# Kernel tuning notes

Hardware: AMD Instinct MI355X
Metric: run time of the kernel (lower is better)

The kernel has to match this reference:

```python
import jax, jax.numpy as jnp
import numpy as np

BETA = 0.25


def setup_inputs() -> dict:
    key = jax.random.key(0)
    k1, k2 = jax.random.split(key)
    inputs = jax.random.normal(k1, (16, 64, 64, 256), dtype=jnp.float32)
    # codebook, shape (embedding_dim=256, num_embeddings=1024), uniform init like tf
    embeddings = jax.random.uniform(k2, (256, 1024), dtype=jnp.float32)
    return {"inputs": inputs, "embeddings": embeddings}


def reference(inputs, embeddings):
    D = embeddings.shape[0]
    flat = inputs.reshape(-1, D)  # [N, D]
    distances = (
        jnp.sum(flat * flat, axis=1, keepdims=True)
        - 2.0 * (flat @ embeddings)
        + jnp.sum(embeddings * embeddings, axis=0, keepdims=True)
    )
    encoding_indices = jnp.argmin(distances, axis=1)  # == argmax(-d)
    # one_hot @ embeddings.T is just a row gather from the codebook
    quantized = jnp.take(embeddings.T, encoding_indices, axis=0).reshape(inputs.shape)
    commitment_loss = BETA * jnp.mean(
        (jax.lax.stop_gradient(quantized) - inputs) ** 2
    )
    # straight-through estimator
    quantized = inputs + jax.lax.stop_gradient(quantized - inputs)
    return quantized, commitment_loss, encoding_indices
```

## Files before the change

kernel.cpp:

```cpp
#include <hip/hip_runtime.h>
#include <float.h>

typedef _Float16 half8 __attribute__((ext_vector_type(8)));
typedef float    f32x4 __attribute__((ext_vector_type(4)));
typedef unsigned long long u64;

#define N_ROWS   65536
#define DIM      256
#define KCODES   1024
#define VQ_BETA  0.25
#define MARGIN   1.5f
#define HCAP     640

__device__ __forceinline__ unsigned fkey(float f) {
    const unsigned u = __float_as_uint(f);
    return u ^ (0x80000000u | (unsigned)((int)u >> 31));
}

__global__ void transpose_e(const float* __restrict__ E, float* __restrict__ Et) {
    __shared__ float t[32][33];
    const int kt = blockIdx.x * 32;
    const int dt = blockIdx.y * 32;
    const int lx = threadIdx.x & 31;
    const int ly = threadIdx.x >> 5;
#pragma unroll
    for (int i = 0; i < 4; ++i) {
        int d = dt + ly + i * 8;
        t[ly + i * 8][lx] = E[(size_t)d * KCODES + kt + lx];
    }
    __syncthreads();
#pragma unroll
    for (int i = 0; i < 4; ++i) {
        int k = kt + ly + i * 8;
        Et[(size_t)k * DIM + dt + lx] = t[lx][ly + i * 8];
    }
}

__global__ void enorm_kernel(const float* __restrict__ E, float* __restrict__ enorm) {
    const int k = blockIdx.x * 256 + threadIdx.x;
    float s = 0.f;
#pragma unroll 4
    for (int d = 0; d < DIM; ++d) {
        float v = E[(size_t)d * KCODES + k];
        s = fmaf(v, v, s);
    }
    enorm[k] = s;
}

__global__ void efrag_kernel(const float* __restrict__ Et, _Float16* __restrict__ Efb) {
    const int fid = blockIdx.x * 256 + threadIdx.x;
    const int lhi   = fid & 3;
    const int llo   = (fid >> 2) & 15;
    const int nt    = (fid >> 6) & 3;
    const int w     = (fid >> 8) & 3;
    const int slice = fid >> 10;
    const int chunk = slice >> 3, ks = slice & 7;
    const int code  = chunk * 256 + w * 64 + nt * 16 + llo;
    const float* src = Et + (size_t)code * DIM + ks * 32 + lhi * 8;
    half8 h;
#pragma unroll
    for (int j = 0; j < 8; ++j) h[j] = (_Float16)src[j];
    *reinterpret_cast<half8*>(Efb + (size_t)fid * 8) = h;
}

__device__ __forceinline__ void load_bf2(const _Float16* __restrict__ eb,
                                         half8 (&bf)[2]) {
    bf[0] = *reinterpret_cast<const half8*>(eb);
    bf[1] = *reinterpret_cast<const half8*>(eb + 512);
}
__device__ __forceinline__ void load_af(const char* AhB, int ks, int llo, int lhi,
                                        int aswz, half8 (&af)[4]) {
#pragma unroll
    for (int mt = 0; mt < 4; ++mt) {
        const int addr = ((mt * 16 + llo) * 512 + (ks * 4 + lhi) * 16) ^ aswz;
        af[mt] = *reinterpret_cast<const half8*>(AhB + addr);
    }
}
__device__ __forceinline__ void mfma_chunk(
        const _Float16* __restrict__ ebase, const char* AhB,
        int llo, int lhi, int aswz, f32x4 (&acc)[4][2]) {
    half8 bf[4][2], af[4];
#pragma unroll
    for (int k = 0; k < 4; ++k) load_bf2(ebase + (size_t)k * 8192, bf[k]);
#pragma unroll
    for (int ks = 0; ks < 8; ++ks) {
        const int b = ks & 3;
        const half8 b0 = bf[b][0], b1 = bf[b][1];
        if (ks < 4) load_bf2(ebase + (size_t)(ks + 4) * 8192, bf[b]);
        load_af(AhB, ks, llo, lhi, aswz, af);
#pragma unroll
        for (int mt = 0; mt < 4; ++mt) {
            acc[mt][0] = __builtin_amdgcn_mfma_f32_16x16x32_f16(af[mt], b0, acc[mt][0], 0, 0, 0);
            acc[mt][1] = __builtin_amdgcn_mfma_f32_16x16x32_f16(af[mt], b1, acc[mt][1], 0, 0, 0);
        }
    }
}

__global__ __launch_bounds__(512, 4) void vq_mfma(
        const float* __restrict__ X, const _Float16* __restrict__ Efb,
        const float* __restrict__ enorm, const float* __restrict__ Et,
        float* __restrict__ outidx, float* __restrict__ outq,
        float* __restrict__ partials)
{
    __shared__ _Float16 Ah[64 * 256];
    __shared__ float    bminw[8][64];
    __shared__ float    cutoff_s[64];
    __shared__ float    rmin_s[64];
    __shared__ u64      minpk[64];
    __shared__ int      rowbad[64];
    __shared__ int      hits[HCAP];
    __shared__ float    xs[DIM];
    __shared__ float    wlsum[8];
    __shared__ unsigned hitcnt;

    const int tid = threadIdx.x;
    const int rowbase = blockIdx.x * 64;

    if (tid == 0) hitcnt = 0;
    if (tid < 64) {
        minpk[tid] = 0xFFFFFFFFFFFFFFFFULL;
        rmin_s[tid] = FLT_MAX;
        rowbad[tid] = 0;
    }

    {
        const int row = tid >> 3;
#pragma unroll
        for (int i = 0; i < 4; ++i) {
            const int g = (tid & 7) + 8 * i;
            const float* src = X + (size_t)(rowbase + row) * DIM + g * 8;
            float4 a = *reinterpret_cast<const float4*>(src);
            float4 b = *reinterpret_cast<const float4*>(src + 4);
            half8 h;
            h[0] = (_Float16)a.x; h[1] = (_Float16)a.y;
            h[2] = (_Float16)a.z; h[3] = (_Float16)a.w;
            h[4] = (_Float16)b.x; h[5] = (_Float16)b.y;
            h[6] = (_Float16)b.z; h[7] = (_Float16)b.w;
            const int addr = (row * 512 + g * 16) ^ ((row & 7) << 4);
            *reinterpret_cast<half8*>(reinterpret_cast<char*>(Ah) + addr) = h;
        }
    }
    __syncthreads();

    const int w    = tid >> 6;
    const int lane = tid & 63;
    const int lhi  = lane >> 4, llo = lane & 15;
    const int aswz = (llo & 7) << 4;
    const int lane_off8 = (llo * 4 + lhi) * 8;
    const char* AhB = reinterpret_cast<const char*>(Ah);

    for (int chunk = 0; chunk < 4; ++chunk) {
        f32x4 acc[4][2];
#pragma unroll
        for (int mt = 0; mt < 4; ++mt)
#pragma unroll
            for (int nt = 0; nt < 2; ++nt) acc[mt][nt] = (f32x4){0.f, 0.f, 0.f, 0.f};

        const _Float16* ebase = Efb + (size_t)chunk * 65536 + w * 1024 + lane_off8;
        mfma_chunk(ebase, AhB, llo, lhi, aswz, acc);

        float e2v[2];
#pragma unroll
        for (int nt = 0; nt < 2; ++nt)
            e2v[nt] = enorm[chunk * 256 + w * 32 + nt * 16 + llo];

        float mloc[16];
#pragma unroll
        for (int mt = 0; mt < 4; ++mt)
#pragma unroll
            for (int q = 0; q < 4; ++q) {
                float m = FLT_MAX;
#pragma unroll
                for (int nt = 0; nt < 2; ++nt) {
                    const float ds = fmaf(-2.0f, acc[mt][nt][q], e2v[nt]);
                    acc[mt][nt][q] = ds;
                    m = fminf(m, ds);
                }
                mloc[mt * 4 + q] = m;
            }
#pragma unroll
        for (int m = 1; m < 16; m <<= 1)
#pragma unroll
            for (int sl = 0; sl < 16; ++sl)
                mloc[sl] = fminf(mloc[sl], __shfl_xor(mloc[sl], m, 64));
        if (llo == 0) {
#pragma unroll
            for (int mt = 0; mt < 4; ++mt)
#pragma unroll
                for (int q = 0; q < 4; ++q)
                    bminw[w][mt * 16 + lhi * 4 + q] = mloc[mt * 4 + q];
        }
        __syncthreads();
        if (tid < 64) {
            float r = bminw[0][tid];
#pragma unroll
            for (int ww = 1; ww < 8; ++ww) r = fminf(r, bminw[ww][tid]);
            r = fminf(rmin_s[tid], r);
            rmin_s[tid]   = r;
            cutoff_s[tid] = r + MARGIN;
        }
        __syncthreads();

#pragma unroll
        for (int mt = 0; mt < 4; ++mt)
#pragma unroll
            for (int q = 0; q < 4; ++q) {
                const int row = mt * 16 + lhi * 4 + q;
                const float cut = cutoff_s[row];
#pragma unroll
                for (int nt = 0; nt < 2; ++nt) {
                    if (acc[mt][nt][q] < cut) {
                        const unsigned p = atomicAdd(&hitcnt, 1u);
                        if (p < HCAP)
                            hits[p] = (row << 10) |
                                      (chunk * 256 + w * 32 + nt * 16 + llo);
                        else
                            rowbad[row] = 1;
                    }
                }
            }
    }
    __syncthreads();

    const int nh = (int)(hitcnt < HCAP ? hitcnt : (unsigned)HCAP);

    for (int hi = tid; hi < nh; hi += 512) {
        const int pk = hits[hi];
        const int rl = pk >> 10, code = pk & 1023;
        const float* xr = X  + (size_t)(rowbase + rl) * DIM;
        const float* er = Et + (size_t)code * DIM;
        float p = 0.f, x2 = 0.f;
#pragma unroll
        for (int j = 0; j < 64; ++j) {
            float4 xv = *reinterpret_cast<const float4*>(xr + j * 4);
            float4 ev = *reinterpret_cast<const float4*>(er + j * 4);
            x2 = fmaf(xv.x, xv.x, x2); x2 = fmaf(xv.y, xv.y, x2);
            x2 = fmaf(xv.z, xv.z, x2); x2 = fmaf(xv.w, xv.w, x2);
            p  = fmaf(xv.x, ev.x, p);  p  = fmaf(xv.y, ev.y, p);
            p  = fmaf(xv.z, ev.z, p);  p  = fmaf(xv.w, ev.w, p);
        }
        const float dd = (x2 - 2.0f * p) + enorm[code];
        atomicMin(&minpk[rl], ((u64)fkey(dd) << 10) | (unsigned)code);
    }
    __syncthreads();

    for (int r = 0; r < 64; ++r) {
        if (!rowbad[r]) continue;
        if (tid < 256) xs[tid] = X[(size_t)(rowbase + r) * DIM + tid];
        __syncthreads();
        if (tid < 256) {
            float x2 = 0.f;
            for (int d = 0; d < DIM; ++d) x2 = fmaf(xs[d], xs[d], x2);
            float a0 = 0.f, a1 = 0.f, a2 = 0.f, a3 = 0.f;
            const float* e0 = Et + (size_t)(tid      ) * DIM;
            const float* e1 = Et + (size_t)(tid + 256) * DIM;
            const float* e2p = Et + (size_t)(tid + 512) * DIM;
            const float* e3 = Et + (size_t)(tid + 768) * DIM;
            for (int d = 0; d < DIM; ++d) {
                const float xv = xs[d];
                a0 = fmaf(xv, e0[d], a0);
                a1 = fmaf(xv, e1[d], a1);
                a2 = fmaf(xv, e2p[d], a2);
                a3 = fmaf(xv, e3[d], a3);
            }
            const float d0 = (x2 - 2.0f * a0) + enorm[tid];
            const float d1 = (x2 - 2.0f * a1) + enorm[tid + 256];
            const float d2 = (x2 - 2.0f * a2) + enorm[tid + 512];
            const float d3 = (x2 - 2.0f * a3) + enorm[tid + 768];
            atomicMin(&minpk[r], ((u64)fkey(d0) << 10) | (unsigned)tid);
            atomicMin(&minpk[r], ((u64)fkey(d1) << 10) | (unsigned)(tid + 256));
            atomicMin(&minpk[r], ((u64)fkey(d2) << 10) | (unsigned)(tid + 512));
            atomicMin(&minpk[r], ((u64)fkey(d3) << 10) | (unsigned)(tid + 768));
        }
        __syncthreads();
    }

    float lsum = 0.f;
    {
        const int row  = tid >> 3;
        const int part = tid & 7;
        const int cw   = (int)(minpk[row] & 1023ULL);
        const float* xrow = X  + (size_t)(rowbase + row) * DIM;
        const float* ew   = Et + (size_t)cw * DIM;
        float* oq = outq + (size_t)(rowbase + row) * DIM;
        if (part == 0) outidx[rowbase + row] = (float)cw;

#pragma unroll
        for (int j = 0; j < 8; ++j) {
            const int d0 = j * 32 + part * 4;
            float4 q = *reinterpret_cast<const float4*>(ew + d0);
            float4 x = *reinterpret_cast<const float4*>(xrow + d0);
            float4 o;
            o.x = x.x + (q.x - x.x);
            o.y = x.y + (q.y - x.y);
            o.z = x.z + (q.z - x.z);
            o.w = x.w + (q.w - x.w);
            *reinterpret_cast<float4*>(oq + d0) = o;
            float dx;
            dx = q.x - x.x; lsum = fmaf(dx, dx, lsum);
            dx = q.y - x.y; lsum = fmaf(dx, dx, lsum);
            dx = q.z - x.z; lsum = fmaf(dx, dx, lsum);
            dx = q.w - x.w; lsum = fmaf(dx, dx, lsum);
        }
    }
#pragma unroll
    for (int m = 1; m < 64; m <<= 1) lsum += __shfl_xor(lsum, m, 64);
    if (lane == 0) wlsum[w] = lsum;
    __syncthreads();
    if (tid == 0) {
        float s = wlsum[0];
#pragma unroll
        for (int ww = 1; ww < 8; ++ww) s += wlsum[ww];
        partials[blockIdx.x] = s;
    }
}

__global__ void loss_final(const float* __restrict__ partials, float* __restrict__ out) {
    __shared__ double sd[256];
    const int tid = threadIdx.x;
    double s = 0.0;
    for (int i = tid; i < 1024; i += 256) s += (double)partials[i];
    sd[tid] = s;
    __syncthreads();
    for (int k = 128; k > 0; k >>= 1) {
        if (tid < k) sd[tid] += sd[tid + k];
        __syncthreads();
    }
    if (tid == 0) out[0] = (float)(VQ_BETA * sd[0] / (double)((size_t)N_ROWS * DIM));
}

extern "C" void kernel_launch(void* const* d_in, const int* in_sizes, int n_in,
                              void* d_out, int out_size, void* d_ws, size_t ws_size,
                              hipStream_t stream) {
    const float* X = (const float*)d_in[0];
    const float* E = (const float*)d_in[1];

    float* outq    = (float*)d_out;
    float* outloss = outq + (size_t)N_ROWS * DIM;
    float* outidx  = outloss + 1;

    float*    Et       = (float*)d_ws;
    _Float16* Efb      = (_Float16*)(Et + 262144);
    float*    enormw   = (float*)(Efb + 262144);
    float*    partials = enormw + KCODES;

    transpose_e <<<dim3(32, 8), 256, 0, stream>>>(E, Et);
    enorm_kernel<<<4,           256, 0, stream>>>(E, enormw);
    efrag_kernel<<<128,         256, 0, stream>>>(Et, Efb);
    vq_mfma     <<<N_ROWS / 64, 512, 0, stream>>>(X, Efb, enormw, Et,
                                                  outidx, outq, partials);
    loss_final  <<<1,           256, 0, stream>>>(partials, outloss);
}
```

Baseline: 164.5 us.

## Fix candidate cutoff from first code chunk and drop per-chunk block reductions

The first 256-code chunk alone now sets each row's cutoff (min distance plus margin), which is cached in registers. The remaining three chunks skip the cross-wave min reduction and its two __syncthreads and filter candidates directly against that fixed cutoff. The enorm loads are also moved ahead of the MFMA loop. The cost is a looser cutoff, since it ignores closer codes found in later chunks, so more hits may be recorded and the HCAP overflow/fallback path may fire more often.

```diff
diff --git a/kernel.cpp b/kernel.cpp
--- a/kernel.cpp
+++ b/kernel.cpp
@@ -105,7 +105,6 @@
     __shared__ _Float16 Ah[64 * 256];
     __shared__ float    bminw[8][64];
     __shared__ float    cutoff_s[64];
-    __shared__ float    rmin_s[64];
     __shared__ u64      minpk[64];
     __shared__ int      rowbad[64];
     __shared__ int      hits[HCAP];
@@ -119,7 +118,6 @@
     if (tid == 0) hitcnt = 0;
     if (tid < 64) {
         minpk[tid] = 0xFFFFFFFFFFFFFFFFULL;
-        rmin_s[tid] = FLT_MAX;
         rowbad[tid] = 0;
     }
 
@@ -149,20 +147,22 @@
     const int lane_off8 = (llo * 4 + lhi) * 8;
     const char* AhB = reinterpret_cast<const char*>(Ah);
 
-    for (int chunk = 0; chunk < 4; ++chunk) {
+    float cut[16];
+
+    {
         f32x4 acc[4][2];
 #pragma unroll
         for (int mt = 0; mt < 4; ++mt)
 #pragma unroll
             for (int nt = 0; nt < 2; ++nt) acc[mt][nt] = (f32x4){0.f, 0.f, 0.f, 0.f};
 
-        const _Float16* ebase = Efb + (size_t)chunk * 65536 + w * 1024 + lane_off8;
+        float e2v[2];
+#pragma unroll
+        for (int nt = 0; nt < 2; ++nt)
+            e2v[nt] = enorm[w * 32 + nt * 16 + llo];
+
+        const _Float16* ebase = Efb + w * 1024 + lane_off8;
         mfma_chunk(ebase, AhB, llo, lhi, aswz, acc);
-
-        float e2v[2];
-#pragma unroll
-        for (int nt = 0; nt < 2; ++nt)
-            e2v[nt] = enorm[chunk * 256 + w * 32 + nt * 16 + llo];
 
         float mloc[16];
 #pragma unroll
@@ -195,21 +195,60 @@
             float r = bminw[0][tid];
 #pragma unroll
             for (int ww = 1; ww < 8; ++ww) r = fminf(r, bminw[ww][tid]);
-            r = fminf(rmin_s[tid], r);
-            rmin_s[tid]   = r;
             cutoff_s[tid] = r + MARGIN;
         }
         __syncthreads();
+
+#pragma unroll
+        for (int mt = 0; mt < 4; ++mt)
+#pragma unroll
+            for (int q = 0; q < 4; ++q)
+                cut[mt * 4 + q] = cutoff_s[mt * 16 + lhi * 4 + q];
 
 #pragma unroll
         for (int mt = 0; mt < 4; ++mt)
 #pragma unroll
             for (int q = 0; q < 4; ++q) {
                 const int row = mt * 16 + lhi * 4 + q;
-                const float cut = cutoff_s[row];
+                const float c = cut[mt * 4 + q];
 #pragma unroll
                 for (int nt = 0; nt < 2; ++nt) {
-                    if (acc[mt][nt][q] < cut) {
+                    if (acc[mt][nt][q] < c) {
+                        const unsigned p = atomicAdd(&hitcnt, 1u);
+                        if (p < HCAP)
+                            hits[p] = (row << 10) | (w * 32 + nt * 16 + llo);
+                        else
+                            rowbad[row] = 1;
+                    }
+                }
+            }
+    }
+
+    for (int chunk = 1; chunk < 4; ++chunk) {
+        f32x4 acc[4][2];
+#pragma unroll
+        for (int mt = 0; mt < 4; ++mt)
+#pragma unroll
+            for (int nt = 0; nt < 2; ++nt) acc[mt][nt] = (f32x4){0.f, 0.f, 0.f, 0.f};
+
+        float e2v[2];
+#pragma unroll
+        for (int nt = 0; nt < 2; ++nt)
+            e2v[nt] = enorm[chunk * 256 + w * 32 + nt * 16 + llo];
+
+        const _Float16* ebase = Efb + (size_t)chunk * 65536 + w * 1024 + lane_off8;
+        mfma_chunk(ebase, AhB, llo, lhi, aswz, acc);
+
+#pragma unroll
+        for (int mt = 0; mt < 4; ++mt)
+#pragma unroll
+            for (int q = 0; q < 4; ++q) {
+                const int row = mt * 16 + lhi * 4 + q;
+                const float c = cut[mt * 4 + q];
+#pragma unroll
+                for (int nt = 0; nt < 2; ++nt) {
+                    const float ds = fmaf(-2.0f, acc[mt][nt][q], e2v[nt]);
+                    if (ds < c) {
                         const unsigned p = atomicAdd(&hitcnt, 1u);
                         if (p < HCAP)
                             hits[p] = (row << 10) |
```

Measured after the change: 291.0 us. 1.77x slower.

## Split quantized-row writeback into separate gather kernel and compute loss from fp16 LDS copy

Applied to the files above, without the earlier changes.

The main kernel no longer re-reads X from global memory or writes the quantized output. It writes the chosen code indices to a workspace buffer and computes the commitment loss from the fp16 copy of the input rows already held in shared memory. A new kernel then gathers the codebook rows into the output using fully coalesced float4 stores. This removes a full re-read of the input from the main kernel, but the loss is now computed against fp16-rounded inputs, which can shift it slightly, and the output now takes an extra launch and its own pass over memory.

```diff
diff --git a/kernel.cpp b/kernel.cpp
--- a/kernel.cpp
+++ b/kernel.cpp
@@ -99,7 +99,7 @@
 __global__ __launch_bounds__(512, 4) void vq_mfma(
         const float* __restrict__ X, const _Float16* __restrict__ Efb,
         const float* __restrict__ enorm, const float* __restrict__ Et,
-        float* __restrict__ outidx, float* __restrict__ outq,
+        float* __restrict__ outidx, int* __restrict__ widx,
         float* __restrict__ partials)
 {
     __shared__ _Float16 Ah[64 * 256];
@@ -280,27 +280,27 @@
         const int row  = tid >> 3;
         const int part = tid & 7;
         const int cw   = (int)(minpk[row] & 1023ULL);
-        const float* xrow = X  + (size_t)(rowbase + row) * DIM;
-        const float* ew   = Et + (size_t)cw * DIM;
-        float* oq = outq + (size_t)(rowbase + row) * DIM;
+        const float* ew = Et + (size_t)cw * DIM;
         if (part == 0) outidx[rowbase + row] = (float)cw;
-
-#pragma unroll
-        for (int j = 0; j < 8; ++j) {
-            const int d0 = j * 32 + part * 4;
-            float4 q = *reinterpret_cast<const float4*>(ew + d0);
-            float4 x = *reinterpret_cast<const float4*>(xrow + d0);
-            float4 o;
-            o.x = x.x + (q.x - x.x);
-            o.y = x.y + (q.y - x.y);
-            o.z = x.z + (q.z - x.z);
-            o.w = x.w + (q.w - x.w);
-            *reinterpret_cast<float4*>(oq + d0) = o;
+        if (part == 1) widx[rowbase + row] = cw;
+
+#pragma unroll
+        for (int i = 0; i < 4; ++i) {
+            const int g = part + 8 * i;
+            const int addr = (row * 512 + g * 16) ^ ((row & 7) << 4);
+            half8 h = *reinterpret_cast<const half8*>(AhB + addr);
+            const int d0 = g * 8;
+            float4 qa = *reinterpret_cast<const float4*>(ew + d0);
+            float4 qb = *reinterpret_cast<const float4*>(ew + d0 + 4);
             float dx;
-            dx = q.x - x.x; lsum = fmaf(dx, dx, lsum);
-            dx = q.y - x.y; lsum = fmaf(dx, dx, lsum);
-            dx = q.z - x.z; lsum = fmaf(dx, dx, lsum);
-            dx = q.w - x.w; lsum = fmaf(dx, dx, lsum);
+            dx = qa.x - (float)h[0]; lsum = fmaf(dx, dx, lsum);
+            dx = qa.y - (float)h[1]; lsum = fmaf(dx, dx, lsum);
+            dx = qa.z - (float)h[2]; lsum = fmaf(dx, dx, lsum);
+            dx = qa.w - (float)h[3]; lsum = fmaf(dx, dx, lsum);
+            dx = qb.x - (float)h[4]; lsum = fmaf(dx, dx, lsum);
+            dx = qb.y - (float)h[5]; lsum = fmaf(dx, dx, lsum);
+            dx = qb.z - (float)h[6]; lsum = fmaf(dx, dx, lsum);
+            dx = qb.w - (float)h[7]; lsum = fmaf(dx, dx, lsum);
         }
     }
 #pragma unroll
@@ -312,6 +312,22 @@
 #pragma unroll
         for (int ww = 1; ww < 8; ++ww) s += wlsum[ww];
         partials[blockIdx.x] = s;
+    }
+}
+
+__global__ __launch_bounds__(256) void quantize_ep(
+        const float* __restrict__ Et, const int* __restrict__ widx,
+        float* __restrict__ outq)
+{
+    const int rowbase = blockIdx.x * 64;
+    const f32x4* Et4 = reinterpret_cast<const f32x4*>(Et);
+    f32x4* out4 = reinterpret_cast<f32x4*>(outq) + (size_t)blockIdx.x * 4096;
+#pragma unroll
+    for (int k = 0; k < 16; ++k) {
+        const int fi  = k * 256 + threadIdx.x;
+        const int row = fi >> 6;
+        const int cw  = widx[rowbase + row];
+        out4[fi] = Et4[(size_t)cw * 64 + (fi & 63)];
     }
 }
 
@@ -343,11 +359,13 @@
     _Float16* Efb      = (_Float16*)(Et + 262144);
     float*    enormw   = (float*)(Efb + 262144);
     float*    partials = enormw + KCODES;
+    int*      widx     = (int*)(partials + 1024);
 
     transpose_e <<<dim3(32, 8), 256, 0, stream>>>(E, Et);
     enorm_kernel<<<4,           256, 0, stream>>>(E, enormw);
     efrag_kernel<<<128,         256, 0, stream>>>(Et, Efb);
     vq_mfma     <<<N_ROWS / 64, 512, 0, stream>>>(X, Efb, enormw, Et,
-                                                  outidx, outq, partials);
+                                                  outidx, widx, partials);
+    quantize_ep <<<N_ROWS / 64, 256, 0, stream>>>(Et, widx, outq);
     loss_final  <<<1,           256, 0, stream>>>(partials, outloss);
 }
```

Result: slower. 180.4 us (+9.7%).
